# Kernel tuning notes

Hardware: AMD Instinct MI355X
Metric: run time of the kernel (lower is better)

## Reference

```python
import jax, jax.numpy as jnp
import numpy as np

# SequentialEdge (torchdrug): for each offset i in [-D, D], connect every atom of
# residue r to every atom of residue r+i within the same graph, keep only pairs on
# the same chain, relation id = i + D. We use a regular batch (B graphs, R residues
# per graph, A atoms per residue) so all shapes are static; edges filtered out by
# the same-chain test are padded with -1 rows (the torch original compacts them,
# which is a data-dependent shape and not jit-expressible).

B, R, A, D = 256, 256, 8, 2  # graphs, residues/graph, atoms/residue, max_distance
N = B * R * A
RTOT = B * R


def setup_inputs() -> dict:
    key = jax.random.key(0)
    atom2residue = jnp.arange(N, dtype=jnp.int32) // A        # [N]
    residue2graph = jnp.arange(RTOT, dtype=jnp.int32) // R    # [RTOT]
    chain_id = jax.random.randint(key, (RTOT,), 0, 4, dtype=jnp.int32)  # 4 chains/graph
    return {
        "chain_id": chain_id,
        "atom2residue": atom2residue,
        "residue2graph": residue2graph,
        "num_graph": B,
        "residues_per_graph": R,
        "atoms_per_residue": A,
        "max_distance": D,
    }


def reference(chain_id, atom2residue, residue2graph, num_graph, residues_per_graph,
              atoms_per_residue, max_distance):
    Bg, Rr, Aa, Dd = num_graph, residues_per_graph, atoms_per_residue, max_distance
    a = jnp.arange(Aa, dtype=jnp.int32)
    g = jnp.arange(Bg, dtype=jnp.int32)
    chunks = []
    for i in range(-Dd, Dd + 1):  # small fixed loop over 2*D+1 relation offsets
        Rv = Rr - abs(i)
        lo = max(0, -i)  # first valid local residue index for node_in
        local_in = jnp.arange(lo, lo + Rv, dtype=jnp.int32)           # [Rv]
        res_in = g[:, None] * Rr + local_in[None, :]                   # [B, Rv] global residue ids
        res_out = res_in + i                                           # partner residue, same graph
        node_in = res_in[..., None] * Aa + a                           # [B, Rv, A]
        node_out = res_out[..., None] * Aa + a                         # [B, Rv, A]
        # variadic_meshgrid order: in-atom varies slowly, out-atom fast, per residue segment
        ni = jnp.broadcast_to(node_in[..., :, None], (Bg, Rv, Aa, Aa)).reshape(-1)
        no = jnp.broadcast_to(node_out[..., None, :], (Bg, Rv, Aa, Aa)).reshape(-1)
        same_chain = chain_id[atom2residue[ni]] == chain_id[atom2residue[no]]
        rel = jnp.full(ni.shape, i + Dd, dtype=jnp.int32)
        edges = jnp.stack([ni, no, rel], axis=-1)                      # [E_i, 3]
        chunks.append(jnp.where(same_chain[:, None], edges, jnp.int32(-1)))
    edge_list = jnp.concatenate(chunks, axis=0)                        # [E_total, 3]
    return edge_list, jnp.int32(2 * Dd + 1)
```

## Files before the change

kernel.cpp:

```cpp
#include <hip/hip_runtime.h>
#include <hip/hip_bf16.h>


#define E_TOTAL   20873216u
#define INT_TOTAL 62619648u
#define NT4       15654912u

__device__ __forceinline__ void decode_edge(unsigned e, const int* __restrict__ ch,
                                            int& x, int& y, int& z) {
    unsigned g, rem;
    int i, lo, rel;
    if (e < 4161536u) {
        unsigned eo = e;
        g = eo / 16256u; rem = eo - g * 16256u; i = -2; lo = 2; rel = 0;
    } else if (e < 8339456u) {
        unsigned eo = e - 4161536u;
        g = eo / 16320u; rem = eo - g * 16320u; i = -1; lo = 1; rel = 1;
    } else if (e < 12533760u) {
        unsigned eo = e - 8339456u;
        g = eo >> 14;    rem = eo & 16383u;     i = 0;  lo = 0; rel = 2;
    } else if (e < 16711680u) {
        unsigned eo = e - 12533760u;
        g = eo / 16320u; rem = eo - g * 16320u; i = 1;  lo = 0; rel = 3;
    } else {
        unsigned eo = e - 16711680u;
        g = eo / 16256u; rem = eo - g * 16256u; i = 2;  lo = 0; rel = 4;
    }
    unsigned rl = (rem >> 6) + (unsigned)lo;
    unsigned ai = (rem >> 3) & 7u;
    unsigned ao = rem & 7u;
    int res_in  = (int)(g * 256u + rl);
    int res_out = res_in + i;
    bool same = (ch[res_in] == ch[res_out]);
    x = same ? res_in  * 8 + (int)ai : -1;
    y = same ? res_out * 8 + (int)ao : -1;
    z = same ? rel : -1;
}

__global__ __launch_bounds__(256)
void seqedge_kernel(const int* __restrict__ chain, int* __restrict__ out) {
    unsigned t = blockIdx.x * 256u + threadIdx.x;
    if (t >= NT4) return;
    unsigned j0 = t * 4u;
    unsigned e0 = j0 / 3u;
    unsigned c0 = j0 - e0 * 3u;
    unsigned e1 = e0 + 1u;
    if (e1 >= E_TOTAL) e1 = E_TOTAL - 1u;

    int x0, y0, z0, x1, y1, z1;
    decode_edge(e0, chain, x0, y0, z0);
    decode_edge(e1, chain, x1, y1, z1);

    int4 v;
    if (c0 == 0u)      v = make_int4(x0, y0, z0, x1);
    else if (c0 == 1u) v = make_int4(y0, z0, x1, y1);
    else               v = make_int4(z0, x1, y1, z1);

    reinterpret_cast<int4*>(out)[t] = v;

    if (t == 0u) out[INT_TOTAL] = 5;
}

extern "C" void kernel_launch(void* const* d_in, const int* in_sizes, int n_in,
                              void* d_out, int out_size, void* d_ws, size_t ws_size,
                              hipStream_t stream) {
    const int* chain_id = (const int*)d_in[0];
    int* out = (int*)d_out;
    const unsigned nthreads = NT4;
    const unsigned nblocks = (nthreads + 255u) / 256u;
    seqedge_kernel<<<nblocks, 256, 0, stream>>>(chain_id, out);
}
```

Measured before the change: 250.2 us.

## Map one wavefront per residue pair with 3D grid and nontemporal stores

Replaces the flat per-int4 decoding, which needed integer divisions and branchy edge-range lookups, with a 3D grid over relation offset, graph and residue. Each wavefront handles one residue pair, loads the two chain ids once and writes its 48 int4 chunks with simple arithmetic. Stores become nontemporal to avoid cache pollution on this pure-write kernel. One quarter of the lanes in each wave sit idle, and some blocks exit early.

```diff
diff --git a/kernel.cpp b/kernel.cpp
--- a/kernel.cpp
+++ b/kernel.cpp
@@ -1,64 +1,55 @@
 #include <hip/hip_runtime.h>
-#include <hip/hip_bf16.h>
 
 
-#define E_TOTAL   20873216u
 #define INT_TOTAL 62619648u
-#define NT4       15654912u
 
-__device__ __forceinline__ void decode_edge(unsigned e, const int* __restrict__ ch,
-                                            int& x, int& y, int& z) {
-    unsigned g, rem;
-    int i, lo, rel;
-    if (e < 4161536u) {
-        unsigned eo = e;
-        g = eo / 16256u; rem = eo - g * 16256u; i = -2; lo = 2; rel = 0;
-    } else if (e < 8339456u) {
-        unsigned eo = e - 4161536u;
-        g = eo / 16320u; rem = eo - g * 16320u; i = -1; lo = 1; rel = 1;
-    } else if (e < 12533760u) {
-        unsigned eo = e - 8339456u;
-        g = eo >> 14;    rem = eo & 16383u;     i = 0;  lo = 0; rel = 2;
-    } else if (e < 16711680u) {
-        unsigned eo = e - 12533760u;
-        g = eo / 16320u; rem = eo - g * 16320u; i = 1;  lo = 0; rel = 3;
-    } else {
-        unsigned eo = e - 16711680u;
-        g = eo / 16256u; rem = eo - g * 16256u; i = 2;  lo = 0; rel = 4;
-    }
-    unsigned rl = (rem >> 6) + (unsigned)lo;
-    unsigned ai = (rem >> 3) & 7u;
-    unsigned ao = rem & 7u;
-    int res_in  = (int)(g * 256u + rl);
-    int res_out = res_in + i;
-    bool same = (ch[res_in] == ch[res_out]);
-    x = same ? res_in  * 8 + (int)ai : -1;
-    y = same ? res_out * 8 + (int)ao : -1;
-    z = same ? rel : -1;
-}
+typedef int iv4 __attribute__((ext_vector_type(4)));
 
 __global__ __launch_bounds__(256)
 void seqedge_kernel(const int* __restrict__ chain, int* __restrict__ out) {
-    unsigned t = blockIdx.x * 256u + threadIdx.x;
-    if (t >= NT4) return;
-    unsigned j0 = t * 4u;
-    unsigned e0 = j0 / 3u;
-    unsigned c0 = j0 - e0 * 3u;
-    unsigned e1 = e0 + 1u;
-    if (e1 >= E_TOTAL) e1 = E_TOTAL - 1u;
+    const int z     = (int)blockIdx.z;
+    const int ioff  = z - 2;
+    const int absio = ioff < 0 ? -ioff : ioff;
+    const int Rv    = 256 - absio;
+    const int lo    = ioff < 0 ? -ioff : 0;
 
-    int x0, y0, z0, x1, y1, z1;
-    decode_edge(e0, chain, x0, y0, z0);
-    decode_edge(e1, chain, x1, y1, z1);
+    static const unsigned base4_tab[5] = {0u, 3121152u, 6254592u, 9400320u, 12533760u};
+    const unsigned base4 = base4_tab[z];
 
-    int4 v;
-    if (c0 == 0u)      v = make_int4(x0, y0, z0, x1);
-    else if (c0 == 1u) v = make_int4(y0, z0, x1, y1);
-    else               v = make_int4(z0, x1, y1, z1);
+    if (threadIdx.x == 0u && blockIdx.x == 0u && blockIdx.y == 0u && blockIdx.z == 0u)
+        out[INT_TOTAL] = 5;
 
-    reinterpret_cast<int4*>(out)[t] = v;
+    const unsigned w  = threadIdx.x >> 6;
+    const int      rv = (int)(blockIdx.x * 4u + w);
+    if (rv >= Rv) return;
 
-    if (t == 0u) out[INT_TOTAL] = 5;
+    const int g       = (int)blockIdx.y;
+    const int res_in  = g * 256 + lo + rv;
+    const int res_out = res_in + ioff;
+    const bool same   = chain[res_in] == chain[res_out];
+
+    const unsigned l = threadIdx.x & 63u;
+    if (l >= 48u) return;
+
+    const unsigned idx4 = base4 + (unsigned)(g * Rv + rv) * 48u + l;
+
+    iv4 v;
+    if (!same) {
+        v = (iv4){-1, -1, -1, -1};
+    } else {
+        const unsigned j0 = l * 4u;
+        const unsigned e0 = j0 / 3u;
+        const unsigned c0 = j0 - e0 * 3u;
+        const unsigned e1 = e0 + 1u;
+        const int ri8 = res_in * 8, ro8 = res_out * 8;
+        const int x0 = ri8 + (int)(e0 >> 3), y0 = ro8 + (int)(e0 & 7u);
+        const int x1 = ri8 + (int)(e1 >> 3), y1 = ro8 + (int)(e1 & 7u);
+        const int rel = z;
+        if (c0 == 0u)      v = (iv4){x0,  y0,  rel, x1 };
+        else if (c0 == 1u) v = (iv4){y0,  rel, x1,  y1 };
+        else               v = (iv4){rel, x1,  y1,  rel};
+    }
+    __builtin_nontemporal_store(v, reinterpret_cast<iv4*>(out) + idx4);
 }
 
 extern "C" void kernel_launch(void* const* d_in, const int* in_sizes, int n_in,
@@ -66,7 +57,6 @@
                               hipStream_t stream) {
     const int* chain_id = (const int*)d_in[0];
     int* out = (int*)d_out;
-    const unsigned nthreads = NT4;
-    const unsigned nblocks = (nthreads + 255u) / 256u;
-    seqedge_kernel<<<nblocks, 256, 0, stream>>>(chain_id, out);
+    dim3 grid(64, 256, 5);
+    seqedge_kernel<<<grid, 256, 0, stream>>>(chain_id, out);
 }
```

Result: slower. 260.2 us (+4.0%).
